# Kernel tuning notes

Measured on AMD Instinct MI355X. Metric: run time of the kernel, lower is better.

## Reference

```python
import jax, jax.numpy as jnp
import numpy as np

NUM_USERS = 100000
NUM_ITEMS = 50000
EMB = 64
N_EDGES = 4800000
N_NODES = NUM_USERS + NUM_ITEMS
NEG_SLOPE = 0.01  # torch F.leaky_relu default


def setup_inputs() -> dict:
    key = jax.random.key(0)
    ks = jax.random.split(key, 12)
    inp = {
        "user_indices": jnp.arange(NUM_USERS, dtype=jnp.int32),
        "item_indices": jnp.arange(NUM_ITEMS, dtype=jnp.int32),
        "adj_rows": jax.random.randint(ks[0], (N_EDGES,), 0, N_NODES, dtype=jnp.int32),
        "adj_cols": jax.random.randint(ks[1], (N_EDGES,), 0, N_NODES, dtype=jnp.int32),
        "adj_vals": jax.random.uniform(ks[2], (N_EDGES,), dtype=jnp.float32),
        "user_emb": jax.random.normal(ks[3], (NUM_USERS, EMB), dtype=jnp.float32),
        "item_emb": jax.random.normal(ks[4], (NUM_ITEMS, EMB), dtype=jnp.float32),
    }
    # two propagation layers (layers=[64,64,64] -> zip gives 2 Linear pairs)
    s = 1.0 / np.sqrt(EMB)
    for li, kb in zip(range(2), range(5, 12, 4)):
        inp[f"W_gc{li}"] = jax.random.uniform(ks[kb], (EMB, EMB), jnp.float32, -s, s)
        inp[f"b_gc{li}"] = jax.random.uniform(ks[kb + 1], (EMB,), jnp.float32, -s, s)
        inp[f"W_bi{li}"] = jax.random.uniform(ks[kb + 2], (EMB, EMB), jnp.float32, -s, s)
        inp[f"b_bi{li}"] = jax.random.uniform(ks[kb + 3], (EMB,), jnp.float32, -s, s)
    return inp


def reference(user_indices, item_indices, adj_rows, adj_cols, adj_vals,
              user_emb, item_emb,
              W_gc0, b_gc0, W_bi0, b_bi0,
              W_gc1, b_gc1, W_bi1, b_bi1):
    ego = jnp.concatenate([user_emb[user_indices], item_emb[item_indices]], axis=0)  # [N, 64]
    n_nodes = ego.shape[0]
    all_embeddings = [ego]
    layer_params = [(W_gc0, b_gc0, W_bi0, b_bi0), (W_gc1, b_gc1, W_bi1, b_bi1)]
    for Wg, bg, Wb, bb in layer_params:
        # sparse adj @ ego : gather by col, scale by val, scatter-add by row
        side = jax.ops.segment_sum(adj_vals[:, None] * ego[adj_cols], adj_rows,
                                   num_segments=n_nodes)  # [N, 64]
        sum_emb = jax.nn.leaky_relu(side @ Wg.T + bg, NEG_SLOPE)
        bi_emb = jax.nn.leaky_relu((ego * side) @ Wb.T + bb, NEG_SLOPE)
        ego = sum_emb + bi_emb
        all_embeddings.append(ego)
    all_embeddings = jnp.concatenate(all_embeddings, axis=1)  # [N, 192]
    n_users = user_indices.shape[0]
    return all_embeddings[:n_users], all_embeddings[n_users:]
```

## Files before the change

kernel.cpp:

```cpp
#include <hip/hip_runtime.h>

#define NUSERS 100000
#define NITEMS 50000
#define NNODES 150000
#define EMB 64
#define NEDGES 4800000
#define OUTC 192
#define NEG_SLOPE 0.01f

#define BKT_SHIFT 10
#define NB 147
#define G 1024
#define EPB 4688
#define NSCAN (NB * G)

typedef __attribute__((ext_vector_type(8))) short bf16x8;
typedef __attribute__((ext_vector_type(4))) float f32x4;

__device__ __forceinline__ unsigned short f2bf(float f) {
    unsigned u = __float_as_uint(f);
    unsigned r = (u + 0x7fffu + ((u >> 16) & 1u)) >> 16;
    return (unsigned short)r;
}
__device__ __forceinline__ float bf2f(short s) {
    return __uint_as_float(((unsigned)(unsigned short)s) << 16);
}

__global__ void build_ego(const int* __restrict__ ui, const int* __restrict__ ii,
                          const float* __restrict__ uemb, const float* __restrict__ iemb,
                          float* __restrict__ out, unsigned short* __restrict__ egoc) {
    int gid = blockIdx.x * blockDim.x + threadIdx.x;
    int r = gid >> 4, p = gid & 15;
    if (r >= NNODES) return;
    const float* src = (r < NUSERS) ? (uemb + (size_t)ui[r] * EMB)
                                    : (iemb + (size_t)ii[r - NUSERS] * EMB);
    float4 v = ((const float4*)src)[p];
    *(float4*)(out + (size_t)r * OUTC + p * 4) = v;
    ushort4 o;
    o.x = f2bf(v.x); o.y = f2bf(v.y); o.z = f2bf(v.z); o.w = f2bf(v.w);
    *(ushort4*)(egoc + (size_t)r * EMB + p * 4) = o;
}

__global__ void conv_w4(const float* __restrict__ s0, const float* __restrict__ s1,
                        const float* __restrict__ s2, const float* __restrict__ s3,
                        unsigned short* __restrict__ d0, unsigned short* __restrict__ d1,
                        unsigned short* __restrict__ d2, unsigned short* __restrict__ d3) {
    int i = blockIdx.x * 256 + threadIdx.x;
    if (i < 4096) {
        d0[i] = f2bf(s0[i]); d1[i] = f2bf(s1[i]);
        d2[i] = f2bf(s2[i]); d3[i] = f2bf(s3[i]);
    }
}

__global__ __launch_bounds__(256) void bucket_hist(const int* __restrict__ rows,
                                                   int* __restrict__ hist) {
    __shared__ int h[NB];
    int tid = threadIdx.x, blk = blockIdx.x;
    if (tid < NB) h[tid] = 0;
    __syncthreads();
    int q0 = blk * (EPB / 4), q1 = q0 + (EPB / 4);
    const int qmax = NEDGES / 4;
    if (q1 > qmax) q1 = qmax;
    for (int q = q0 + tid; q < q1; q += 256) {
        int4 r4 = ((const int4*)rows)[q];
        atomicAdd(&h[r4.x >> BKT_SHIFT], 1);
        atomicAdd(&h[r4.y >> BKT_SHIFT], 1);
        atomicAdd(&h[r4.z >> BKT_SHIFT], 1);
        atomicAdd(&h[r4.w >> BKT_SHIFT], 1);
    }
    __syncthreads();
    if (tid < NB) hist[(size_t)tid * G + blk] = h[tid];
}

__global__ void scan_chunk(const int* __restrict__ counts, int* __restrict__ outp,
                           int* __restrict__ blksum, int n) {
    __shared__ int buf[1024];
    int tid = threadIdx.x;
    int gid = blockIdx.x * 1024 + tid;
    int v = (gid < n) ? counts[gid] : 0;
    buf[tid] = v;
    __syncthreads();
    for (int off = 1; off < 1024; off <<= 1) {
        int t = (tid >= off) ? buf[tid - off] : 0;
        __syncthreads();
        buf[tid] += t;
        __syncthreads();
    }
    if (gid < n) outp[gid + 1] = buf[tid];
    if (tid == 1023) blksum[blockIdx.x] = buf[tid];
}

__global__ void scan_sums(int* __restrict__ blksum, int n) {
    __shared__ int buf[256];
    int tid = threadIdx.x;
    int v = (tid < n) ? blksum[tid] : 0;
    buf[tid] = v;
    __syncthreads();
    for (int off = 1; off < 256; off <<= 1) {
        int t = (tid >= off) ? buf[tid - off] : 0;
        __syncthreads();
        buf[tid] += t;
        __syncthreads();
    }
    if (tid < n) blksum[tid] = buf[tid] - v;
}

__global__ void add_offsets(int* __restrict__ outp, const int* __restrict__ blksum, int n) {
    int gid = blockIdx.x * 1024 + threadIdx.x;
    if (gid < n) outp[gid + 1] += blksum[blockIdx.x];
    if (gid == 0) outp[0] = 0;
}

__global__ __launch_bounds__(256) void bucket_scatter(
        const int* __restrict__ rows, const int* __restrict__ cols,
        const float* __restrict__ vals, const int* __restrict__ base,
        int2* __restrict__ bedge) {
    __shared__ int cur[NB];
    int tid = threadIdx.x, blk = blockIdx.x;
    if (tid < NB) cur[tid] = base[(size_t)tid * G + blk];
    __syncthreads();
    int q0 = blk * (EPB / 4), q1 = q0 + (EPB / 4);
    const int qmax = NEDGES / 4;
    if (q1 > qmax) q1 = qmax;
    for (int q = q0 + tid; q < q1; q += 256) {
        int4   r4 = ((const int4*)rows)[q];
        int4   c4 = ((const int4*)cols)[q];
        float4 v4 = ((const float4*)vals)[q];
        int s0 = atomicAdd(&cur[r4.x >> BKT_SHIFT], 1);
        bedge[s0] = make_int2(c4.x | ((r4.x & 1023) << 18), __float_as_int(v4.x));
        int s1 = atomicAdd(&cur[r4.y >> BKT_SHIFT], 1);
        bedge[s1] = make_int2(c4.y | ((r4.y & 1023) << 18), __float_as_int(v4.y));
        int s2 = atomicAdd(&cur[r4.z >> BKT_SHIFT], 1);
        bedge[s2] = make_int2(c4.z | ((r4.z & 1023) << 18), __float_as_int(v4.z));
        int s3 = atomicAdd(&cur[r4.w >> BKT_SHIFT], 1);
        bedge[s3] = make_int2(c4.w | ((r4.w & 1023) << 18), __float_as_int(v4.w));
    }
}

__global__ __launch_bounds__(1024) void bucket_csr(
        const int2* __restrict__ bedge, const int* __restrict__ base,
        int* __restrict__ rowptr, int2* __restrict__ csr) {
    __shared__ int h[1024];
    __shared__ int h2[1024];
    int tid = threadIdx.x, bkt = blockIdx.x;
    int s  = base[(size_t)bkt * G];
    int e2 = base[(size_t)(bkt + 1) * G];
    h[tid] = 0;
    __syncthreads();
    for (int i = s + tid; i < e2; i += 1024)
        atomicAdd(&h[(unsigned)bedge[i].x >> 18], 1);
    __syncthreads();
    int v = h[tid];
    h2[tid] = v;
    __syncthreads();
    for (int off = 1; off < 1024; off <<= 1) {
        int t = (tid >= off) ? h2[tid - off] : 0;
        __syncthreads();
        h2[tid] += t;
        __syncthreads();
    }
    int excl = s + h2[tid] - v;
    int rbase = bkt << BKT_SHIFT;
    if (rbase + tid < NNODES) rowptr[rbase + tid] = excl;
    if (bkt == NB - 1 && tid == 0) rowptr[NNODES] = NEDGES;
    h[tid] = excl;
    __syncthreads();
    for (int i = s + tid; i < e2; i += 1024) {
        int2 t = bedge[i];
        int slot = atomicAdd(&h[(unsigned)t.x >> 18], 1);
        csr[slot] = make_int2(t.x & 0x3FFFF, t.y);
    }
}

#define ACC8(g, v)                                              \
    a0 = fmaf(v, __uint_as_float((g).x << 16), a0);             \
    a1 = fmaf(v, __uint_as_float((g).x & 0xffff0000u), a1);     \
    a2 = fmaf(v, __uint_as_float((g).y << 16), a2);             \
    a3 = fmaf(v, __uint_as_float((g).y & 0xffff0000u), a3);     \
    a4 = fmaf(v, __uint_as_float((g).z << 16), a4);             \
    a5 = fmaf(v, __uint_as_float((g).z & 0xffff0000u), a5);     \
    a6 = fmaf(v, __uint_as_float((g).w << 16), a6);             \
    a7 = fmaf(v, __uint_as_float((g).w & 0xffff0000u), a7);

__global__ __launch_bounds__(512) void spmm_gather(
        const int* __restrict__ rowptr, const int2* __restrict__ csr,
        const unsigned short* __restrict__ egoc,
        unsigned short* __restrict__ sideb,
        int strideE) {
    int tid = blockIdx.x * blockDim.x + threadIdx.x;
    int row = tid >> 3;
    int dg  = tid & 7;
    if (row >= NNODES) return;
    int lane = threadIdx.x & 63;
    int g0l  = lane & ~7;
    int s = rowptr[row], e = rowptr[row + 1];
    const uint4* egc = (const uint4*)egoc;
    float a0 = 0.f, a1 = 0.f, a2 = 0.f, a3 = 0.f,
          a4 = 0.f, a5 = 0.f, a6 = 0.f, a7 = 0.f;
    for (int b = s; b < e; b += 8) {
        int idx = b + dg;
        int2 cv = csr[idx < e ? idx : (e - 1)];
        float vv = (idx < e) ? __int_as_float(cv.y) : 0.f;
        int   c0 = __shfl(cv.x, g0l + 0); float v0 = __shfl(vv, g0l + 0);
        int   c1 = __shfl(cv.x, g0l + 1); float v1 = __shfl(vv, g0l + 1);
        int   c2 = __shfl(cv.x, g0l + 2); float v2 = __shfl(vv, g0l + 2);
        int   c3 = __shfl(cv.x, g0l + 3); float v3 = __shfl(vv, g0l + 3);
        int   c4 = __shfl(cv.x, g0l + 4); float v4 = __shfl(vv, g0l + 4);
        int   c5 = __shfl(cv.x, g0l + 5); float v5 = __shfl(vv, g0l + 5);
        int   c6 = __shfl(cv.x, g0l + 6); float v6 = __shfl(vv, g0l + 6);
        int   c7 = __shfl(cv.x, g0l + 7); float v7 = __shfl(vv, g0l + 7);
        uint4 g0 = egc[(size_t)c0 * 8 + dg];
        uint4 g1 = egc[(size_t)c1 * 8 + dg];
        uint4 g2 = egc[(size_t)c2 * 8 + dg];
        uint4 g3 = egc[(size_t)c3 * 8 + dg];
        uint4 g4 = egc[(size_t)c4 * 8 + dg];
        uint4 g5 = egc[(size_t)c5 * 8 + dg];
        uint4 g6 = egc[(size_t)c6 * 8 + dg];
        uint4 g7 = egc[(size_t)c7 * 8 + dg];
        ACC8(g0, v0); ACC8(g1, v1); ACC8(g2, v2); ACC8(g3, v3);
        ACC8(g4, v4); ACC8(g5, v5); ACC8(g6, v6); ACC8(g7, v7);
    }
    uint p0 = (unsigned)f2bf(a0) | ((unsigned)f2bf(a1) << 16);
    uint p1 = (unsigned)f2bf(a2) | ((unsigned)f2bf(a3) << 16);
    uint p2 = (unsigned)f2bf(a4) | ((unsigned)f2bf(a5) << 16);
    uint p3 = (unsigned)f2bf(a6) | ((unsigned)f2bf(a7) << 16);
    uint4 st = make_uint4(p0, p1, p2, p3);
    *(uint4*)(sideb + (size_t)row * strideE + dg * 8) = st;
}

__global__ __launch_bounds__(256) void dense_mfma(
        const unsigned short* __restrict__ sideb, int sStrideE,
        const unsigned short* __restrict__ egoc,
        const unsigned short* __restrict__ wg,
        const unsigned short* __restrict__ wb,
        const float* __restrict__ bg, const float* __restrict__ bb,
        float* __restrict__ outCol,
        unsigned short* __restrict__ egocNew) {
    int lane = threadIdx.x & 63;
    int ct   = (threadIdx.x >> 6) * 16;
    int rtile = blockIdx.x * 16;
    int ar = lane & 15, kg = lane >> 4;
    bf16x8 sfrag[2], pfrag[2], wgf[2], wbf[2];
    #pragma unroll
    for (int t = 0; t < 2; ++t) {
        int koff = kg * 8 + 32 * t;
        bf16x8 sv = *(const bf16x8*)(sideb + (size_t)(rtile + ar) * sStrideE + koff);
        bf16x8 ev = *(const bf16x8*)(egoc  + (size_t)(rtile + ar) * EMB + koff);
        sfrag[t] = sv;
        bf16x8 pv;
        #pragma unroll
        for (int j = 0; j < 8; ++j)
            pv[j] = (short)f2bf(bf2f(sv[j]) * bf2f(ev[j]));
        pfrag[t] = pv;
        wgf[t] = *(const bf16x8*)(wg + (size_t)(ct + ar) * EMB + koff);
        wbf[t] = *(const bf16x8*)(wb + (size_t)(ct + ar) * EMB + koff);
    }
    f32x4 accg = {0.f, 0.f, 0.f, 0.f}, accb = {0.f, 0.f, 0.f, 0.f};
    accg = __builtin_amdgcn_mfma_f32_16x16x32_bf16(sfrag[0], wgf[0], accg, 0, 0, 0);
    accg = __builtin_amdgcn_mfma_f32_16x16x32_bf16(sfrag[1], wgf[1], accg, 0, 0, 0);
    accb = __builtin_amdgcn_mfma_f32_16x16x32_bf16(pfrag[0], wbf[0], accb, 0, 0, 0);
    accb = __builtin_amdgcn_mfma_f32_16x16x32_bf16(pfrag[1], wbf[1], accb, 0, 0, 0);
    int c = ct + ar;
    float biasg = bg[c], biasb = bb[c];
    #pragma unroll
    for (int i = 0; i < 4; ++i) {
        int r = rtile + kg * 4 + i;
        float g = accg[i] + biasg; g = (g > 0.f) ? g : NEG_SLOPE * g;
        float q = accb[i] + biasb; q = (q > 0.f) ? q : NEG_SLOPE * q;
        float nv = g + q;
        outCol[(size_t)r * OUTC + c] = nv;
        if (egocNew) egocNew[(size_t)r * EMB + c] = f2bf(nv);
    }
}

extern "C" void kernel_launch(void* const* d_in, const int* in_sizes, int n_in,
                              void* d_out, int out_size, void* d_ws, size_t ws_size,
                              hipStream_t stream) {
    const int*   ui   = (const int*)  d_in[0];
    const int*   ii   = (const int*)  d_in[1];
    const int*   rows = (const int*)  d_in[2];
    const int*   cols = (const int*)  d_in[3];
    const float* vals = (const float*)d_in[4];
    const float* uemb = (const float*)d_in[5];
    const float* iemb = (const float*)d_in[6];
    const float* Wg0 = (const float*)d_in[7],  *bg0 = (const float*)d_in[8];
    const float* Wb0 = (const float*)d_in[9],  *bb0 = (const float*)d_in[10];
    const float* Wg1 = (const float*)d_in[11], *bg1 = (const float*)d_in[12];
    const float* Wb1 = (const float*)d_in[13], *bb1 = (const float*)d_in[14];
    float* out = (float*)d_out;

    char* ws = (char*)d_ws;
    int2*  csr    = (int2*)ws; ws += (size_t)NEDGES * 8;
    char*  buf0   = ws;        ws += (size_t)NNODES * EMB * 2;
    char*  buf1   = ws;        ws += (size_t)NNODES * EMB * 2;
    unsigned short* egoc0 = (unsigned short*)ws; ws += (size_t)NNODES * EMB * 2;
    int*   rowptr = (int*) ws; ws += (size_t)(NNODES + 1) * 4;
    int*   hist   = (int*) ws; ws += (size_t)NSCAN * 4;
    int*   scanb  = (int*) ws; ws += (size_t)(NSCAN + 1) * 4;
    int*   blksum = (int*) ws; ws += 256 * 4;
    unsigned short* wgb0 = (unsigned short*)ws; ws += 4096 * 2;
    unsigned short* wbb0 = (unsigned short*)ws; ws += 4096 * 2;
    unsigned short* wgb1 = (unsigned short*)ws; ws += 4096 * 2;
    unsigned short* wbb1 = (unsigned short*)ws; ws += 4096 * 2;
    int2* bedge = (int2*)buf0;
    unsigned short* egoc1 = (unsigned short*)buf1;

    build_ego<<<(NNODES * 16 + 255) / 256, 256, 0, stream>>>(ui, ii, uemb, iemb,
                                                             out, egoc0);
    conv_w4<<<16, 256, 0, stream>>>(Wg0, Wb0, Wg1, Wb1, wgb0, wbb0, wgb1, wbb1);

    bucket_hist<<<G, 256, 0, stream>>>(rows, hist);
    scan_chunk<<<NSCAN / 1024, 1024, 0, stream>>>(hist, scanb, blksum, NSCAN);
    scan_sums<<<1, 256, 0, stream>>>(blksum, NSCAN / 1024);
    add_offsets<<<NSCAN / 1024, 1024, 0, stream>>>(scanb, blksum, NSCAN);
    bucket_scatter<<<G, 256, 0, stream>>>(rows, cols, vals, scanb, bedge);
    bucket_csr<<<NB, 1024, 0, stream>>>(bedge, scanb, rowptr, csr);

    unsigned short* side0 = (unsigned short*)((char*)out + 512);
    const int SIDE0_STRIDE = 384;
    spmm_gather<<<(NNODES * 8 + 511) / 512, 512, 0, stream>>>(rowptr, csr, egoc0,
                                                              side0, SIDE0_STRIDE);
    dense_mfma<<<NNODES / 16, 256, 0, stream>>>(side0, SIDE0_STRIDE, egoc0,
                                                wgb0, wbb0, bg0, bb0,
                                                out + 64, egoc1);

    unsigned short* side1 = (unsigned short*)buf0;
    spmm_gather<<<(NNODES * 8 + 511) / 512, 512, 0, stream>>>(rowptr, csr, egoc1,
                                                              side1, EMB);
    dense_mfma<<<NNODES / 16, 256, 0, stream>>>(side1, EMB, egoc1,
                                                wgb1, wbb1, bg1, bb1,
                                                out + 128, (unsigned short*)nullptr);
}
```

Before: 410.0 us.

## Sort CSR edges by column slice within rows and simplify gather loop

```diff
diff --git a/kernel.cpp b/kernel.cpp
--- a/kernel.cpp
+++ b/kernel.cpp
@@ -13,6 +13,9 @@
 #define G 1024
 #define EPB 4688
 #define NSCAN (NB * G)
+#define NSLICE 10
+#define SLICE_SHIFT 14
+#define NBINS (1024 * NSLICE)
 
 typedef __attribute__((ext_vector_type(8))) short bf16x8;
 typedef __attribute__((ext_vector_type(4))) float f32x4;
@@ -140,34 +143,43 @@
 __global__ __launch_bounds__(1024) void bucket_csr(
         const int2* __restrict__ bedge, const int* __restrict__ base,
         int* __restrict__ rowptr, int2* __restrict__ csr) {
-    __shared__ int h[1024];
-    __shared__ int h2[1024];
+    __shared__ int h[NBINS];
+    __shared__ int tsum[1024];
     int tid = threadIdx.x, bkt = blockIdx.x;
     int s  = base[(size_t)bkt * G];
     int e2 = base[(size_t)(bkt + 1) * G];
-    h[tid] = 0;
-    __syncthreads();
-    for (int i = s + tid; i < e2; i += 1024)
-        atomicAdd(&h[(unsigned)bedge[i].x >> 18], 1);
-    __syncthreads();
-    int v = h[tid];
-    h2[tid] = v;
+    for (int i = tid; i < NBINS; i += 1024) h[i] = 0;
+    __syncthreads();
+    for (int i = s + tid; i < e2; i += 1024) {
+        int x = bedge[i].x;
+        int bin = (x >> 18) * NSLICE + (((unsigned)x & 0x3FFFFu) >> SLICE_SHIFT);
+        atomicAdd(&h[bin], 1);
+    }
+    __syncthreads();
+    int b0 = tid * NSLICE;
+    int cnt[NSLICE];
+    int run = 0;
+    #pragma unroll
+    for (int i = 0; i < NSLICE; ++i) { cnt[i] = h[b0 + i]; run += cnt[i]; }
+    tsum[tid] = run;
     __syncthreads();
     for (int off = 1; off < 1024; off <<= 1) {
-        int t = (tid >= off) ? h2[tid - off] : 0;
-        __syncthreads();
-        h2[tid] += t;
-        __syncthreads();
-    }
-    int excl = s + h2[tid] - v;
+        int t = (tid >= off) ? tsum[tid - off] : 0;
+        __syncthreads();
+        tsum[tid] += t;
+        __syncthreads();
+    }
+    int excl = s + tsum[tid] - run;
     int rbase = bkt << BKT_SHIFT;
     if (rbase + tid < NNODES) rowptr[rbase + tid] = excl;
     if (bkt == NB - 1 && tid == 0) rowptr[NNODES] = NEDGES;
-    h[tid] = excl;
+    #pragma unroll
+    for (int i = 0; i < NSLICE; ++i) { int c = cnt[i]; h[b0 + i] = excl; excl += c; }
     __syncthreads();
     for (int i = s + tid; i < e2; i += 1024) {
         int2 t = bedge[i];
-        int slot = atomicAdd(&h[(unsigned)t.x >> 18], 1);
+        int bin = (t.x >> 18) * NSLICE + (((unsigned)t.x & 0x3FFFFu) >> SLICE_SHIFT);
+        int slot = atomicAdd(&h[bin], 1);
         csr[slot] = make_int2(t.x & 0x3FFFF, t.y);
     }
 }
@@ -191,34 +203,24 @@
     int row = tid >> 3;
     int dg  = tid & 7;
     if (row >= NNODES) return;
-    int lane = threadIdx.x & 63;
-    int g0l  = lane & ~7;
     int s = rowptr[row], e = rowptr[row + 1];
     const uint4* egc = (const uint4*)egoc;
     float a0 = 0.f, a1 = 0.f, a2 = 0.f, a3 = 0.f,
           a4 = 0.f, a5 = 0.f, a6 = 0.f, a7 = 0.f;
-    for (int b = s; b < e; b += 8) {
-        int idx = b + dg;
-        int2 cv = csr[idx < e ? idx : (e - 1)];
-        float vv = (idx < e) ? __int_as_float(cv.y) : 0.f;
-        int   c0 = __shfl(cv.x, g0l + 0); float v0 = __shfl(vv, g0l + 0);
-        int   c1 = __shfl(cv.x, g0l + 1); float v1 = __shfl(vv, g0l + 1);
-        int   c2 = __shfl(cv.x, g0l + 2); float v2 = __shfl(vv, g0l + 2);
-        int   c3 = __shfl(cv.x, g0l + 3); float v3 = __shfl(vv, g0l + 3);
-        int   c4 = __shfl(cv.x, g0l + 4); float v4 = __shfl(vv, g0l + 4);
-        int   c5 = __shfl(cv.x, g0l + 5); float v5 = __shfl(vv, g0l + 5);
-        int   c6 = __shfl(cv.x, g0l + 6); float v6 = __shfl(vv, g0l + 6);
-        int   c7 = __shfl(cv.x, g0l + 7); float v7 = __shfl(vv, g0l + 7);
-        uint4 g0 = egc[(size_t)c0 * 8 + dg];
-        uint4 g1 = egc[(size_t)c1 * 8 + dg];
-        uint4 g2 = egc[(size_t)c2 * 8 + dg];
-        uint4 g3 = egc[(size_t)c3 * 8 + dg];
-        uint4 g4 = egc[(size_t)c4 * 8 + dg];
-        uint4 g5 = egc[(size_t)c5 * 8 + dg];
-        uint4 g6 = egc[(size_t)c6 * 8 + dg];
-        uint4 g7 = egc[(size_t)c7 * 8 + dg];
+    for (int b = s; b < e; b += 4) {
+        int i1 = b + 1 < e ? b + 1 : e - 1;
+        int i2 = b + 2 < e ? b + 2 : e - 1;
+        int i3 = b + 3 < e ? b + 3 : e - 1;
+        int2 cv0 = csr[b], cv1 = csr[i1], cv2 = csr[i2], cv3 = csr[i3];
+        float v0 = __int_as_float(cv0.y);
+        float v1 = (b + 1 < e) ? __int_as_float(cv1.y) : 0.f;
+        float v2 = (b + 2 < e) ? __int_as_float(cv2.y) : 0.f;
+        float v3 = (b + 3 < e) ? __int_as_float(cv3.y) : 0.f;
+        uint4 g0 = egc[(size_t)cv0.x * 8 + dg];
+        uint4 g1 = egc[(size_t)cv1.x * 8 + dg];
+        uint4 g2 = egc[(size_t)cv2.x * 8 + dg];
+        uint4 g3 = egc[(size_t)cv3.x * 8 + dg];
         ACC8(g0, v0); ACC8(g1, v1); ACC8(g2, v2); ACC8(g3, v3);
-        ACC8(g4, v4); ACC8(g5, v5); ACC8(g6, v6); ACC8(g7, v7);
     }
     uint p0 = (unsigned)f2bf(a0) | ((unsigned)f2bf(a1) << 16);
     uint p1 = (unsigned)f2bf(a2) | ((unsigned)f2bf(a3) << 16);
```

After: 407.5 us. About the same (-0.6%).
